# Optimization experiments

Measured on AMD Instinct MI355X. Metric: run time of the kernel, lower is better.

The kernel has to match this reference:

```python
import jax, jax.numpy as jnp
import numpy as np

V_TH = 1.0

def spike_fn(x):
    # Heaviside spike (surrogate gradient only matters for bwd)
    return (x > 0).astype(x.dtype)

def setup_inputs() -> dict:
    key = jax.random.key(0)
    ks = jax.random.split(key, 7)
    B, T, I = 256, 512, 512
    H, NB, O = 1024, 4, 128
    HB = H // NB
    x = jax.random.normal(ks[0], (B, T, I), dtype=jnp.float32)
    v0 = jax.random.uniform(ks[1], (B, H), dtype=jnp.float32)  # torch.rand init
    W_branch = jax.random.normal(ks[2], (NB, I, HB), dtype=jnp.float32) * (1.0 / np.sqrt(I))
    tau_n = jax.random.uniform(ks[3], (NB, HB), minval=2.0, maxval=6.0, dtype=jnp.float32)
    tau_m = jax.random.uniform(ks[4], (H,), minval=0.0, maxval=4.0, dtype=jnp.float32)
    W_out = jax.random.normal(ks[5], (H, O), dtype=jnp.float32) * (1.0 / np.sqrt(H))
    b_out = jnp.zeros((O,), dtype=jnp.float32)
    return {"x": x, "v0": v0, "W_branch": W_branch, "tau_n": tau_n,
            "tau_m": tau_m, "W_out": W_out, "b_out": b_out}

def reference(x, v0, W_branch, tau_n, tau_m, W_out, b_out):
    B, T, I = x.shape
    NB, _, HB = W_branch.shape
    H = NB * HB
    beta = jax.nn.sigmoid(tau_n)[:, None, :]   # (NB, 1, HB)
    alpha = jax.nn.sigmoid(tau_m)              # (H,)
    xt = jnp.transpose(x, (1, 0, 2))           # (T, B, I)
    mask = (jnp.arange(T) >= T // 2).astype(x.dtype)  # integrate 2nd half only

    def step(carry, inp):
        d, v, s, acc = carry
        x_t, m = inp
        branch_in = jnp.einsum('bi,nio->nbo', x_t, W_branch)  # (NB, B, HB)
        d = beta * d + (1.0 - beta) * branch_in
        total = jnp.transpose(d, (1, 0, 2)).reshape(B, H)      # cat branches dim=1
        v = alpha * v + (1.0 - alpha) * total - V_TH * s
        s = spike_fn(v - V_TH)
        acc = acc + s * m
        return (d, v, s, acc), None

    d0 = jnp.zeros((NB, B, HB), dtype=x.dtype)
    s0 = jnp.zeros((B, H), dtype=x.dtype)
    acc0 = jnp.zeros((B, H), dtype=x.dtype)
    (d, v, s, acc), _ = jax.lax.scan(step, (d0, v0, s0, acc0), (xt, mask))
    return acc @ W_out + b_out
```

## Files before the change

kernel.cpp:

```cpp
#include <hip/hip_runtime.h>
#include <hip/hip_bf16.h>

#define BSZ 256
#define TT  512
#define II  512
#define HH  1024
#define OO  128
#define BH  262144

typedef short bfrag8 __attribute__((ext_vector_type(8)));
typedef float f32x4  __attribute__((ext_vector_type(4)));

__device__ __forceinline__ unsigned short f2bf(float f) {
    union { float f; unsigned int u; } c; c.f = f;
    unsigned int u = c.u;
    unsigned int r = u + 0x7fffu + ((u >> 16) & 1u);
    return (unsigned short)(r >> 16);
}
__device__ __forceinline__ float bf2f(unsigned short h) {
    union { unsigned int u; float f; } c; c.u = ((unsigned int)h) << 16;
    return c.f;
}

__device__ __forceinline__ void pack2(float f0, float f1, int& hi, int& lo) {
    __hip_bfloat162 h2 = __float22bfloat162_rn(make_float2(f0, f1));
    float r0 = f0 - __bfloat162float(h2.x);
    float r1 = f1 - __bfloat162float(h2.y);
    __hip_bfloat162 l2 = __float22bfloat162_rn(make_float2(r0, r1));
    union { __hip_bfloat162 b; int i; } ch, cl;
    ch.b = h2; cl.b = l2;
    hi = ch.i; lo = cl.i;
}

__device__ __forceinline__ void split8(f32x4 a, f32x4 b, bfrag8& hi, bfrag8& lo) {
    union { bfrag8 v; int i[4]; } H, L;
    pack2(a.x, a.y, H.i[0], L.i[0]);
    pack2(a.z, a.w, H.i[1], L.i[1]);
    pack2(b.x, b.y, H.i[2], L.i[2]);
    pack2(b.z, b.w, H.i[3], L.i[3]);
    hi = H.v; lo = L.v;
}

__global__ __launch_bounds__(256) void setup_k(const float* __restrict__ Wb,
                                               const float* __restrict__ v0,
                                               unsigned short* __restrict__ Whi,
                                               unsigned short* __restrict__ Wlo,
                                               float* __restrict__ dS, float* __restrict__ vS,
                                               float* __restrict__ sS, float* __restrict__ aS) {
    int idx = blockIdx.x * 256 + threadIdx.x;
    int n = idx >> 17;
    int rem = idx & 131071;
    int i = rem >> 8;
    int o = rem & 255;
    int h = (n << 8) + o;
    float w = Wb[idx];
    unsigned short hi = f2bf(w);
    float fh = bf2f(hi);
    unsigned short lo = f2bf(w - fh);
    Whi[(size_t)h * II + i] = hi;
    Wlo[(size_t)h * II + i] = lo;
    if (idx < BH) {
        dS[idx] = 0.0f; vS[idx] = v0[idx]; sS[idx] = 0.0f; aS[idx] = 0.0f;
    }
}

#define GLL16(G, Lp) __builtin_amdgcn_global_load_lds(                         \
    (const __attribute__((address_space(1))) void*)(G),                        \
    (__attribute__((address_space(3))) void*)(Lp), 16, 0, 0)

#define BAR() do { asm volatile("" ::: "memory");                              \
                   __builtin_amdgcn_s_barrier();                               \
                   asm volatile("" ::: "memory"); } while (0)

#define STAGE(K0, BUFB) do {                                                   \
    _Pragma("unroll") for (int j_ = 0; j_ < 4; ++j_) {                         \
        int w8_ = (j_ << 3) + wv;                                              \
        GLL16(gA + (K0) + ((size_t)w8_ << 12), smem + (BUFB) + (w8_ << 10));   \
        GLL16(gB + (K0) + ((size_t)w8_ << 12), smem + (BUFB) + 32768 + (w8_ << 10)); \
    } } while (0)

#define LOADA2(F, BUFB, H0, L0, H1, L1) do {                                   \
    const char* p_ = smem + (BUFB) + aRow + ((F) << 11);                       \
    f32x4 x0_ = *(const f32x4*)(p_ + aO0);                                     \
    f32x4 x1_ = *(const f32x4*)(p_ + aO1);                                     \
    f32x4 x2_ = *(const f32x4*)(p_ + 2048 + aO0);                              \
    f32x4 x3_ = *(const f32x4*)(p_ + 2048 + aO1);                              \
    split8(x0_, x1_, H0, L0);                                                  \
    split8(x2_, x3_, H1, L1);                                                  \
} while (0)

#define LOADB(BUFB) do {                                                       \
    const char* p_ = smem + (BUFB) + bRow;                                     \
    _Pragma("unroll") for (int g_ = 0; g_ < 4; ++g_) {                         \
        bh[g_] = *(const bfrag8*)(p_ + (g_ << 11) + bO0);                      \
        bl[g_] = *(const bfrag8*)(p_ + (g_ << 11) + bO1);                      \
    } } while (0)

#define MFMA3(AH, AL, BHG, BLG, C) do {                                        \
    C = __builtin_amdgcn_mfma_f32_16x16x32_bf16(AH, BHG, C, 0, 0, 0);          \
    C = __builtin_amdgcn_mfma_f32_16x16x32_bf16(AH, BLG, C, 0, 0, 0);          \
    C = __builtin_amdgcn_mfma_f32_16x16x32_bf16(AL, BHG, C, 0, 0, 0);          \
} while (0)

#define MM2(F, H0, L0, H1, L1) do {                                            \
    __builtin_amdgcn_s_setprio(1);                                             \
    _Pragma("unroll") for (int g_ = 0; g_ < 4; ++g_) {                         \
        MFMA3(H0, L0, bh[g_], bl[g_], acc[F][g_]);                             \
        MFMA3(H1, L1, bh[g_], bl[g_], acc[(F) + 1][g_]);                       \
    }                                                                          \
    __builtin_amdgcn_s_setprio(0);                                             \
} while (0)

__global__ __launch_bounds__(512, 2) void gemm8(const float* __restrict__ X,
    const unsigned short* __restrict__ Whi, const unsigned short* __restrict__ Wlo,
    float* __restrict__ U)
{
    extern __shared__ char smem[];

    const int P = blockIdx.x;
    const int L = ((P & 7) << 8) | (P >> 3);
    const int m0 = (L >> 2) << 8;
    const int h0 = (L & 3) << 8;

    const int tid = threadIdx.x;
    const int lane = tid & 63;
    const int wv = tid >> 6;
    const int l16 = lane & 15;
    const int q = lane >> 4;
    const int wm = wv >> 2, wn = wv & 3;

    const int e = l16 & 7;
    const int aRow = ((wm << 7) + l16) << 7;
    const int aO0 = ((((q << 1)    ) ^ e) << 4);
    const int aO1 = ((((q << 1) | 1) ^ e) << 4);
    const int bRow = (((wn << 6) + l16) << 7) + 32768;
    const int bO0 = (((q    ) ^ e) << 4);
    const int bO1 = (((q + 4) ^ e) << 4);

    const int rl = lane >> 3;
    const int sp = (lane & 7) ^ (rl & 7);
    const float* gA = X + ((size_t)(m0 + rl) << 9) + (sp << 2);
    const unsigned short* gB = (sp < 4)
        ? (Whi + ((size_t)(h0 + rl) << 9) + (sp << 3))
        : (Wlo + ((size_t)(h0 + rl) << 9) + ((sp - 4) << 3));

    f32x4 acc[8][4];
#pragma unroll
    for (int i = 0; i < 8; ++i)
#pragma unroll
        for (int j = 0; j < 4; ++j)
#pragma unroll
            for (int r = 0; r < 4; ++r) acc[i][j][r] = 0.0f;

    bfrag8 a0h, a0l, a1h, a1l;
    bfrag8 b0h, b0l, b1h, b1l;
    bfrag8 bh[4], bl[4];

    STAGE(0, 0);
    STAGE(32, 65536);
    asm volatile("s_waitcnt vmcnt(8)" ::: "memory");
    __builtin_amdgcn_s_barrier();
    asm volatile("" ::: "memory");
    LOADA2(0, 0, a0h, a0l, a1h, a1l);

#pragma unroll 1
    for (int tt = 0; tt < 16; tt += 2) {
        const int k2 = (tt << 5) + 64;
        LOADB(0);
        LOADA2(2, 0, b0h, b0l, b1h, b1l);
        MM2(0, a0h, a0l, a1h, a1l);
        BAR();
        LOADA2(4, 0, a0h, a0l, a1h, a1l);
        MM2(2, b0h, b0l, b1h, b1l);
        BAR();
        LOADA2(6, 0, b0h, b0l, b1h, b1l);
        MM2(4, a0h, a0l, a1h, a1l);
        asm volatile("s_waitcnt vmcnt(0) lgkmcnt(0)" ::: "memory");
        BAR();
        if (tt < 14) STAGE(k2, 0);
        LOADA2(0, 65536, a0h, a0l, a1h, a1l);
        MM2(6, b0h, b0l, b1h, b1l);
        BAR();
        LOADB(65536);
        LOADA2(2, 65536, b0h, b0l, b1h, b1l);
        MM2(0, a0h, a0l, a1h, a1l);
        BAR();
        LOADA2(4, 65536, a0h, a0l, a1h, a1l);
        MM2(2, b0h, b0l, b1h, b1l);
        BAR();
        LOADA2(6, 65536, b0h, b0l, b1h, b1l);
        MM2(4, a0h, a0l, a1h, a1l);
        asm volatile("s_waitcnt vmcnt(0) lgkmcnt(0)" ::: "memory");
        BAR();
        if (tt < 13) STAGE(k2 + 32, 65536);
        if (tt < 14) LOADA2(0, 0, a0h, a0l, a1h, a1l);
        MM2(6, b0h, b0l, b1h, b1l);
        BAR();
    }

#pragma unroll
    for (int f = 0; f < 8; ++f) {
        const int rb = m0 + (wm << 7) + (f << 4) + (q << 2);
#pragma unroll
        for (int rr = 0; rr < 4; ++rr) {
            const int m = rb + rr;
            const size_t base =
                (((size_t)((m & 511) << 8) + (m >> 9)) << 10) + h0 + (wn << 6) + l16;
#pragma unroll
            for (int g = 0; g < 4; ++g) U[base + (g << 4)] = acc[f][g][rr];
        }
    }
}

__global__ __launch_bounds__(256) void scan_chunk(const float* __restrict__ U,
    const float* __restrict__ tau_n, const float* __restrict__ tau_m,
    float* __restrict__ dS, float* __restrict__ vS,
    float* __restrict__ sS, float* __restrict__ aS, int t0, int Tc)
{
    int idx = blockIdx.x * 256 + threadIdx.x;
    int h = idx & (HH - 1);
    float beta  = 1.0f / (1.0f + __expf(-tau_n[h]));
    float alpha = 1.0f / (1.0f + __expf(-tau_m[h]));
    float ob = 1.0f - beta, oa = 1.0f - alpha;
    float dd = dS[idx], vv = vS[idx], ss = sS[idx], aa = aS[idx];
    const float* Up = U + idx;

    float u[16];
#pragma unroll
    for (int j = 0; j < 16; ++j) u[j] = Up[(size_t)j << 18];

    int tg = 0;
    for (; tg + 16 < Tc; tg += 16) {
#pragma unroll
        for (int j = 0; j < 16; ++j) {
            float uu = u[j];
            u[j] = Up[(size_t)(tg + 16 + j) << 18];
            float msk = ((t0 + tg + j) >= (TT / 2)) ? 1.0f : 0.0f;
            dd = beta * dd + ob * uu;
            vv = alpha * vv + oa * dd - ss;
            ss = (vv > 1.0f) ? 1.0f : 0.0f;
            aa += msk * ss;
        }
    }
#pragma unroll
    for (int j = 0; j < 16; ++j) {
        float uu = u[j];
        float msk = ((t0 + tg + j) >= (TT / 2)) ? 1.0f : 0.0f;
        dd = beta * dd + ob * uu;
        vv = alpha * vv + oa * dd - ss;
        ss = (vv > 1.0f) ? 1.0f : 0.0f;
        aa += msk * ss;
    }
    dS[idx] = dd; vS[idx] = vv; sS[idx] = ss; aS[idx] = aa;
}

__global__ __launch_bounds__(256) void out_gemm(const float* __restrict__ acc,
    const float* __restrict__ Wout, const float* __restrict__ bout,
    float* __restrict__ out)
{
    __shared__ float a_s[HH];
    __shared__ float partial[OO];
    int b = blockIdx.x;
    int o = threadIdx.x & (OO - 1);
    int half = threadIdx.x >> 7;
    for (int i = threadIdx.x; i < HH; i += 256) a_s[i] = acc[b * HH + i];
    __syncthreads();
    float sum = half ? 0.0f : bout[o];
    const float* Wp = Wout + (size_t)half * 512 * OO + o;
    const float* ap = a_s + half * 512;
#pragma unroll 8
    for (int h = 0; h < 512; ++h) sum = fmaf(ap[h], Wp[(size_t)h * OO], sum);
    if (half) partial[o] = sum;
    __syncthreads();
    if (!half) out[b * OO + o] = sum + partial[o];
}

extern "C" void kernel_launch(void* const* d_in, const int* in_sizes, int n_in,
                              void* d_out, int out_size, void* d_ws, size_t ws_size,
                              hipStream_t stream) {
    const float* x     = (const float*)d_in[0];
    const float* v0    = (const float*)d_in[1];
    const float* Wb    = (const float*)d_in[2];
    const float* tau_n = (const float*)d_in[3];
    const float* tau_m = (const float*)d_in[4];
    const float* Wout  = (const float*)d_in[5];
    const float* bout  = (const float*)d_in[6];
    float* out = (float*)d_out;

    char* ws = (char*)d_ws;
    unsigned short* Whi = (unsigned short*)(ws);
    unsigned short* Wlo = (unsigned short*)(ws + (1ll << 20));
    float* dS = (float*)(ws + (2ll << 20));
    float* vS = (float*)(ws + (3ll << 20));
    float* sS = (float*)(ws + (4ll << 20));
    float* aS = (float*)(ws + (5ll << 20));
    float* U  = (float*)(ws + (6ll << 20));

    hipFuncSetAttribute((const void*)gemm8,
                        hipFuncAttributeMaxDynamicSharedMemorySize, 131072);

    setup_k<<<2048, 256, 0, stream>>>(Wb, v0, Whi, Wlo, dS, vS, sS, aS);
    gemm8<<<2048, 512, 131072, stream>>>(x, Whi, Wlo, U);
    scan_chunk<<<BH / 256, 256, 0, stream>>>(U, tau_n, tau_m, dS, vS, sS, aS, 0, TT);
    out_gemm<<<BSZ, 256, 0, stream>>>(aS, Wout, bout, out);
}
```

Baseline: 962.3 us.

## Pre-split X into bf16 hi/lo, chunk time into two GEMM+scan passes, overlap staging

A new kernel converts x into bf16 hi/lo planes once, so the GEMM loads pre-split bf16 fragments from LDS and no longer splits fp32 values inside the main loop. The time dimension is processed in two chunks of 256 steps, each with its own GEMM and scan launch, which halves the size of the U intermediate. Global-to-LDS staging now overlaps the last MFMA block, using vmcnt(8) waits instead of full drains. The cost is an extra pass over x that writes two bf16 copies, plus more kernel launches.

```diff
diff --git a/kernel.cpp b/kernel.cpp
--- a/kernel.cpp
+++ b/kernel.cpp
@@ -7,6 +7,7 @@
 #define HH  1024
 #define OO  128
 #define BH  262144
+#define TC  256
 
 typedef short bfrag8 __attribute__((ext_vector_type(8)));
 typedef float f32x4  __attribute__((ext_vector_type(4)));
@@ -30,15 +31,6 @@
     union { __hip_bfloat162 b; int i; } ch, cl;
     ch.b = h2; cl.b = l2;
     hi = ch.i; lo = cl.i;
-}
-
-__device__ __forceinline__ void split8(f32x4 a, f32x4 b, bfrag8& hi, bfrag8& lo) {
-    union { bfrag8 v; int i[4]; } H, L;
-    pack2(a.x, a.y, H.i[0], L.i[0]);
-    pack2(a.z, a.w, H.i[1], L.i[1]);
-    pack2(b.x, b.y, H.i[2], L.i[2]);
-    pack2(b.z, b.w, H.i[3], L.i[3]);
-    hi = H.v; lo = L.v;
 }
 
 __global__ __launch_bounds__(256) void setup_k(const float* __restrict__ Wb,
@@ -64,6 +56,21 @@
     }
 }
 
+__global__ __launch_bounds__(256) void split_x(const float* __restrict__ X,
+    unsigned short* __restrict__ Xhi, unsigned short* __restrict__ Xlo)
+{
+    size_t idx = ((size_t)blockIdx.x * 256 + threadIdx.x) << 3;
+    f32x4 v0 = *(const f32x4*)(X + idx);
+    f32x4 v1 = *(const f32x4*)(X + idx + 4);
+    union { uint4 v; int i[4]; } H, L;
+    pack2(v0.x, v0.y, H.i[0], L.i[0]);
+    pack2(v0.z, v0.w, H.i[1], L.i[1]);
+    pack2(v1.x, v1.y, H.i[2], L.i[2]);
+    pack2(v1.z, v1.w, H.i[3], L.i[3]);
+    *(uint4*)(Xhi + idx) = H.v;
+    *(uint4*)(Xlo + idx) = L.v;
+}
+
 #define GLL16(G, Lp) __builtin_amdgcn_global_load_lds(                         \
     (const __attribute__((address_space(1))) void*)(G),                        \
     (__attribute__((address_space(3))) void*)(Lp), 16, 0, 0)
@@ -79,21 +86,19 @@
         GLL16(gB + (K0) + ((size_t)w8_ << 12), smem + (BUFB) + 32768 + (w8_ << 10)); \
     } } while (0)
 
-#define LOADA2(F, BUFB, H0, L0, H1, L1) do {                                   \
+#define LDA2(F, BUFB, H0, L0, H1, L1) do {                                     \
     const char* p_ = smem + (BUFB) + aRow + ((F) << 11);                       \
-    f32x4 x0_ = *(const f32x4*)(p_ + aO0);                                     \
-    f32x4 x1_ = *(const f32x4*)(p_ + aO1);                                     \
-    f32x4 x2_ = *(const f32x4*)(p_ + 2048 + aO0);                              \
-    f32x4 x3_ = *(const f32x4*)(p_ + 2048 + aO1);                              \
-    split8(x0_, x1_, H0, L0);                                                  \
-    split8(x2_, x3_, H1, L1);                                                  \
+    H0 = *(const bfrag8*)(p_ + sH);                                            \
+    L0 = *(const bfrag8*)(p_ + sL);                                            \
+    H1 = *(const bfrag8*)(p_ + 2048 + sH);                                     \
+    L1 = *(const bfrag8*)(p_ + 2048 + sL);                                     \
 } while (0)
 
 #define LOADB(BUFB) do {                                                       \
     const char* p_ = smem + (BUFB) + bRow;                                     \
     _Pragma("unroll") for (int g_ = 0; g_ < 4; ++g_) {                         \
-        bh[g_] = *(const bfrag8*)(p_ + (g_ << 11) + bO0);                      \
-        bl[g_] = *(const bfrag8*)(p_ + (g_ << 11) + bO1);                      \
+        bh[g_] = *(const bfrag8*)(p_ + (g_ << 11) + sH);                       \
+        bl[g_] = *(const bfrag8*)(p_ + (g_ << 11) + sL);                       \
     } } while (0)
 
 #define MFMA3(AH, AL, BHG, BLG, C) do {                                        \
@@ -111,14 +116,15 @@
     __builtin_amdgcn_s_setprio(0);                                             \
 } while (0)
 
-__global__ __launch_bounds__(512, 2) void gemm8(const float* __restrict__ X,
+__global__ __launch_bounds__(512, 2) void gemm8(
+    const unsigned short* __restrict__ Xhi, const unsigned short* __restrict__ Xlo,
     const unsigned short* __restrict__ Whi, const unsigned short* __restrict__ Wlo,
-    float* __restrict__ U)
+    float* __restrict__ U, int xrow0)
 {
     extern __shared__ char smem[];
 
     const int P = blockIdx.x;
-    const int L = ((P & 7) << 8) | (P >> 3);
+    const int L = ((P & 7) << 7) | (P >> 3);
     const int m0 = (L >> 2) << 8;
     const int h0 = (L & 3) << 8;
 
@@ -130,16 +136,17 @@
     const int wm = wv >> 2, wn = wv & 3;
 
     const int e = l16 & 7;
+    const int sH = ((q ^ e) << 4);
+    const int sL = (((q + 4) ^ e) << 4);
     const int aRow = ((wm << 7) + l16) << 7;
-    const int aO0 = ((((q << 1)    ) ^ e) << 4);
-    const int aO1 = ((((q << 1) | 1) ^ e) << 4);
     const int bRow = (((wn << 6) + l16) << 7) + 32768;
-    const int bO0 = (((q    ) ^ e) << 4);
-    const int bO1 = (((q + 4) ^ e) << 4);
 
     const int rl = lane >> 3;
-    const int sp = (lane & 7) ^ (rl & 7);
-    const float* gA = X + ((size_t)(m0 + rl) << 9) + (sp << 2);
+    const int sp = (lane & 7) ^ rl;
+    const int grow0 = (m0 << 1) + xrow0;
+    const unsigned short* gA = (sp < 4)
+        ? (Xhi + ((size_t)(grow0 + rl) << 9) + (sp << 3))
+        : (Xlo + ((size_t)(grow0 + rl) << 9) + ((sp - 4) << 3));
     const unsigned short* gB = (sp < 4)
         ? (Whi + ((size_t)(h0 + rl) << 9) + (sp << 3))
         : (Wlo + ((size_t)(h0 + rl) << 9) + ((sp - 4) << 3));
@@ -161,40 +168,51 @@
     asm volatile("s_waitcnt vmcnt(8)" ::: "memory");
     __builtin_amdgcn_s_barrier();
     asm volatile("" ::: "memory");
-    LOADA2(0, 0, a0h, a0l, a1h, a1l);
+    LDA2(0, 0, a0h, a0l, a1h, a1l);
 
 #pragma unroll 1
     for (int tt = 0; tt < 16; tt += 2) {
         const int k2 = (tt << 5) + 64;
         LOADB(0);
-        LOADA2(2, 0, b0h, b0l, b1h, b1l);
+        LDA2(2, 0, b0h, b0l, b1h, b1l);
         MM2(0, a0h, a0l, a1h, a1l);
         BAR();
-        LOADA2(4, 0, a0h, a0l, a1h, a1l);
+        LDA2(4, 0, a0h, a0l, a1h, a1l);
         MM2(2, b0h, b0l, b1h, b1l);
         BAR();
-        LOADA2(6, 0, b0h, b0l, b1h, b1l);
+        LDA2(6, 0, b0h, b0l, b1h, b1l);
         MM2(4, a0h, a0l, a1h, a1l);
-        asm volatile("s_waitcnt vmcnt(0) lgkmcnt(0)" ::: "memory");
-        BAR();
-        if (tt < 14) STAGE(k2, 0);
-        LOADA2(0, 65536, a0h, a0l, a1h, a1l);
-        MM2(6, b0h, b0l, b1h, b1l);
+        asm volatile("s_waitcnt lgkmcnt(0)" ::: "memory");
+        BAR();
+        if (tt < 14) {
+            STAGE(k2, 0);
+            MM2(6, b0h, b0l, b1h, b1l);
+            asm volatile("s_waitcnt vmcnt(8)" ::: "memory");
+        } else {
+            MM2(6, b0h, b0l, b1h, b1l);
+            asm volatile("s_waitcnt vmcnt(0)" ::: "memory");
+        }
+        LDA2(0, 65536, a0h, a0l, a1h, a1l);
         BAR();
         LOADB(65536);
-        LOADA2(2, 65536, b0h, b0l, b1h, b1l);
+        LDA2(2, 65536, b0h, b0l, b1h, b1l);
         MM2(0, a0h, a0l, a1h, a1l);
         BAR();
-        LOADA2(4, 65536, a0h, a0l, a1h, a1l);
+        LDA2(4, 65536, a0h, a0l, a1h, a1l);
         MM2(2, b0h, b0l, b1h, b1l);
         BAR();
-        LOADA2(6, 65536, b0h, b0l, b1h, b1l);
+        LDA2(6, 65536, b0h, b0l, b1h, b1l);
         MM2(4, a0h, a0l, a1h, a1l);
-        asm volatile("s_waitcnt vmcnt(0) lgkmcnt(0)" ::: "memory");
-        BAR();
-        if (tt < 13) STAGE(k2 + 32, 65536);
-        if (tt < 14) LOADA2(0, 0, a0h, a0l, a1h, a1l);
-        MM2(6, b0h, b0l, b1h, b1l);
+        asm volatile("s_waitcnt lgkmcnt(0)" ::: "memory");
+        BAR();
+        if (tt < 13) {
+            STAGE(k2 + 32, 65536);
+            MM2(6, b0h, b0l, b1h, b1l);
+            asm volatile("s_waitcnt vmcnt(8)" ::: "memory");
+            LDA2(0, 0, a0h, a0l, a1h, a1l);
+        } else {
+            MM2(6, b0h, b0l, b1h, b1l);
+        }
         BAR();
     }
 
@@ -205,7 +223,7 @@
         for (int rr = 0; rr < 4; ++rr) {
             const int m = rb + rr;
             const size_t base =
-                (((size_t)((m & 511) << 8) + (m >> 9)) << 10) + h0 + (wn << 6) + l16;
+                (((size_t)((m & 255) << 8) + (m >> 8)) << 10) + h0 + (wn << 6) + l16;
 #pragma unroll
             for (int g = 0; g < 4; ++g) U[base + (g << 4)] = acc[f][g][rr];
         }
@@ -294,13 +312,19 @@
     float* vS = (float*)(ws + (3ll << 20));
     float* sS = (float*)(ws + (4ll << 20));
     float* aS = (float*)(ws + (5ll << 20));
-    float* U  = (float*)(ws + (6ll << 20));
+    unsigned short* Xhi = (unsigned short*)(ws + (6ll << 20));
+    unsigned short* Xlo = (unsigned short*)(ws + (134ll << 20));
+    float* U  = (float*)(ws + (262ll << 20));
 
     hipFuncSetAttribute((const void*)gemm8,
                         hipFuncAttributeMaxDynamicSharedMemorySize, 131072);
 
     setup_k<<<2048, 256, 0, stream>>>(Wb, v0, Whi, Wlo, dS, vS, sS, aS);
-    gemm8<<<2048, 512, 131072, stream>>>(x, Whi, Wlo, U);
-    scan_chunk<<<BH / 256, 256, 0, stream>>>(U, tau_n, tau_m, dS, vS, sS, aS, 0, TT);
+    split_x<<<32768, 256, 0, stream>>>(x, Xhi, Xlo);
+
+    for (int t0 = 0; t0 < TT; t0 += TC) {
+        gemm8<<<1024, 512, 131072, stream>>>(Xhi, Xlo, Whi, Wlo, U, t0);
+        scan_chunk<<<BH / 256, 256, 0, stream>>>(U, tau_n, tau_m, dS, vS, sS, aS, t0, TC);
+    }
     out_gemm<<<BSZ, 256, 0, stream>>>(aS, Wout, bout, out);
 }
```

Result: faster. 936.9 us (-2.6%).
